# Optimization experiments

Measured on AMD Instinct MI355X. Metric: run time of the kernel, lower is better.

## Reference

```python
import jax, jax.numpy as jnp
import numpy as np

N = 100_000      # nodes in batched candidate graph
P = 150_000      # undirected bonds
E = 2 * P        # directed edges; edge 2i=(u,v), 2i+1=(v,u)
M = 10_000       # tree messages scattered onto edges
DN, DE, DM, DX = 256, 64, 256, 256
ITERS = 3


def setup_inputs() -> dict:
    key = jax.random.key(0)
    ks = jax.random.split(key, 12)
    f_node = jax.random.normal(ks[0], (N, DN), jnp.float32)
    f_edge = jax.random.normal(ks[1], (E, DE), jnp.float32)
    src_p = jax.random.randint(ks[2], (P,), 0, N, dtype=jnp.int32)
    dst_p = jax.random.randint(ks[3], (P,), 0, N, dtype=jnp.int32)
    edge_src = jnp.stack([src_p, dst_p], axis=1).reshape(-1)  # [E]
    edge_dst = jnp.stack([dst_p, src_p], axis=1).reshape(-1)  # [E]
    tree_msg = jax.random.normal(ks[4], (M, DM), jnp.float32)
    tree_tgt = (jnp.arange(M, dtype=jnp.int32) * (E // M))    # unique target edge ids
    s = lambda d: np.float32(1.0 / np.sqrt(d))
    W1 = jax.random.normal(ks[5], (DN, DM), jnp.float32) * s(DN)
    W2 = jax.random.normal(ks[6], (DE, DM), jnp.float32) * s(DE)
    W3 = jax.random.normal(ks[7], (DM, DM), jnp.float32) * s(DM)
    b1 = jnp.zeros((DM,), jnp.float32)
    W4 = jax.random.normal(ks[8], (DN, DX), jnp.float32) * s(DN)
    W5 = jax.random.normal(ks[9], (DM, DX), jnp.float32) * s(DM)
    b2 = jnp.zeros((DX,), jnp.float32)
    return dict(f_node=f_node, f_edge=f_edge, tree_msg=tree_msg,
                W1=W1, W2=W2, W3=W3, b1=b1, W4=W4, W5=W5, b2=b2,
                edge_src=edge_src, edge_dst=edge_dst, tree_tgt=tree_tgt)


def reference(f_node, f_edge, tree_msg, W1, W2, W3, b1, W4, W5, b2,
              edge_src, edge_dst, tree_tgt):
    n_nodes = f_node.shape[0]
    n_edges = f_edge.shape[0]
    d_msg = W3.shape[0]
    # scatter tree messages into per-edge alpha (edata['alpha'])
    alpha = jnp.zeros((n_edges, d_msg), f_node.dtype).at[tree_tgt].set(tree_msg)
    # g1_G static part: W1 f_src + W2 f_edge + b1 (constant across iterations)
    base = f_node[edge_src] @ W1 + f_edge @ W2 + b1  # [E, DM]
    rev = jnp.arange(n_edges) ^ 1  # reverse edge of e (pairs stored consecutively)
    msg = jnp.zeros((n_edges, d_msg), f_node.dtype)
    for _ in range(ITERS):
        # line-graph (backtracking=False) copy_src + sum reduce:
        # sum over incoming edges (w,u) of e=(u,v) excluding w==v
        agg = jax.ops.segment_sum(msg, edge_dst, num_segments=n_nodes)  # [N, DM]
        sum_msg = agg[edge_src] - msg[rev]
        msg = jax.nn.relu(base + (sum_msg + alpha) @ W3)
    # readout: copy_edge + sum per destination node, then g2_G
    node_sum = jax.ops.segment_sum(msg, edge_dst, num_segments=n_nodes)  # [N, DM]
    x = jax.nn.relu(f_node @ W4 + node_sum @ W5 + b2)  # [N, DX]
    return x
```

## Files before the change

### kernel.cpp

```cpp
#include <hip/hip_runtime.h>
#include <hip/hip_bf16.h>

typedef __hip_bfloat16 bf16;
typedef __bf16 bf16x8 __attribute__((ext_vector_type(8)));
typedef __bf16 bf16x4 __attribute__((ext_vector_type(4)));
typedef float f32x4 __attribute__((ext_vector_type(4)));

#define DN_ 256
#define DE_ 64
#define DM_ 256
#define DX_ 256
#define LDA1 264
#define LDA2 72
#define CAP 32


static __device__ __forceinline__ bf16 f2b(float x) { return __float2bfloat16(x); }
static __device__ __forceinline__ float us2f(unsigned short u) {
    return __uint_as_float((unsigned)u << 16);
}

union U16x8 { uint4 u; unsigned short s[8]; };

static __device__ __forceinline__ f32x4 mfma16(bf16x8 a, bf16x8 b, f32x4 c) {
    return __builtin_amdgcn_mfma_f32_16x16x32_bf16(a, b, c, 0, 0, 0);
}

template <int LDA, int KTOT>
static __device__ __forceinline__ void gemm_acc(const bf16* T, const bf16* WT,
                                                f32x4 acc[4][4], int lane, int wave) {
    const int m = lane & 15, quad = lane >> 4;
#pragma unroll
    for (int k0 = 0; k0 < KTOT; k0 += 32) {
        bf16x8 a[4], b[4];
#pragma unroll
        for (int i = 0; i < 4; ++i)
            a[i] = *(const bf16x8*)&T[(i * 16 + m) * LDA + k0 + quad * 8];
#pragma unroll
        for (int j = 0; j < 4; ++j) {
            int n = wave * 64 + j * 16 + m;
            b[j] = *(const bf16x8*)&WT[(size_t)n * KTOT + k0 + quad * 8];
        }
#pragma unroll
        for (int i = 0; i < 4; ++i)
#pragma unroll
            for (int j = 0; j < 4; ++j)
                acc[i][j] = mfma16(b[j], a[i], acc[i][j]);
    }
}

__global__ void __launch_bounds__(256) k_transpose(const float* __restrict__ W,
                                                   bf16* __restrict__ WT, int K, int NC) {
    int i = blockIdx.x * 256 + threadIdx.x;
    if (i < K * NC) {
        int k = i / NC, n = i % NC;
        WT[n * K + k] = f2b(W[i]);
    }
}

__global__ void __launch_bounds__(256) k_cvt(const float* __restrict__ in,
                                             bf16* __restrict__ out, long total) {
    long i = ((long)blockIdx.x * 256 + threadIdx.x) * 8;
    if (i >= total) return;
    float4 v0 = *(const float4*)(in + i);
    float4 v1 = *(const float4*)(in + i + 4);
    bf16x8 b = {(__bf16)v0.x, (__bf16)v0.y, (__bf16)v0.z, (__bf16)v0.w,
                (__bf16)v1.x, (__bf16)v1.y, (__bf16)v1.z, (__bf16)v1.w};
    *(bf16x8*)(out + i) = b;
}

__global__ void __launch_bounds__(256) k_bucket(const int* __restrict__ edst,
                                                int* __restrict__ cnt,
                                                int* __restrict__ slot, int E) {
    int e = blockIdx.x * 256 + threadIdx.x;
    if (e < E) {
        int d = edst[e];
        int pos = atomicAdd(&cnt[d], 1);
        if (pos < CAP) slot[(size_t)d * CAP + pos] = e;
    }
}

__global__ void __launch_bounds__(256) k_invset(const int* __restrict__ tgt,
                                                int* __restrict__ inv, int M) {
    int r = blockIdx.x * 256 + threadIdx.x;
    if (r < M) inv[tgt[r]] = r;
}

__global__ void __launch_bounds__(256) k_aggregate(const bf16* __restrict__ msg,
                                                   const int* __restrict__ cnt,
                                                   const int* __restrict__ slot,
                                                   bf16* __restrict__ agg, int N,
                                                   int relu_in) {
    int wid = (blockIdx.x * 256 + threadIdx.x) >> 6;
    int lane = threadIdx.x & 63;
    if (wid >= N) return;
    int c = cnt[wid];
    if (c > CAP) c = CAP;
    const int* sp = slot + (size_t)wid * CAP;
    float a0 = 0.f, a1 = 0.f, a2 = 0.f, a3 = 0.f;
    if (relu_in) {
        for (int i = 0; i < c; ++i) {
            int e = sp[i];
            ushort4 mv = *(const ushort4*)((const unsigned short*)msg + (size_t)e * DM_ + lane * 4);
            a0 += fmaxf(us2f(mv.x), 0.f); a1 += fmaxf(us2f(mv.y), 0.f);
            a2 += fmaxf(us2f(mv.z), 0.f); a3 += fmaxf(us2f(mv.w), 0.f);
        }
    } else {
        for (int i = 0; i < c; ++i) {
            int e = sp[i];
            ushort4 mv = *(const ushort4*)((const unsigned short*)msg + (size_t)e * DM_ + lane * 4);
            a0 += us2f(mv.x); a1 += us2f(mv.y); a2 += us2f(mv.z); a3 += us2f(mv.w);
        }
    }
    bf16x4 o = {(__bf16)a0, (__bf16)a1, (__bf16)a2, (__bf16)a3};
    *(bf16x4*)(agg + (size_t)wid * DM_ + lane * 4) = o;
}

__global__ void __launch_bounds__(256) k_alpha(const float* __restrict__ tm,
                                               const bf16* __restrict__ W3T,
                                               bf16* __restrict__ alpha3, int M) {
    __shared__ bf16 T[64 * LDA1];
    const int tile0 = blockIdx.x * 64, tid = threadIdx.x;
#pragma unroll
    for (int it = 0; it < 16; ++it) {
        int c = tid + it * 256;
        int r = c >> 6, cc = c & 63;
        int row = tile0 + r;
        if (row >= M) row = 0;
        float4 v = *(const float4*)(tm + (size_t)row * DM_ + cc * 4);
        bf16x4 b = {(__bf16)v.x, (__bf16)v.y, (__bf16)v.z, (__bf16)v.w};
        *(bf16x4*)&T[r * LDA1 + cc * 4] = b;
    }
    __syncthreads();
    const int lane = tid & 63, wave = tid >> 6;
    const int m = lane & 15, quad = lane >> 4;
    f32x4 acc[4][4];
#pragma unroll
    for (int i = 0; i < 4; ++i)
#pragma unroll
        for (int j = 0; j < 4; ++j) acc[i][j] = (f32x4){0.f, 0.f, 0.f, 0.f};
    gemm_acc<LDA1, 256>(T, W3T, acc, lane, wave);
#pragma unroll
    for (int i = 0; i < 4; ++i) {
        int row = tile0 + i * 16 + m;
        if (row < M) {
            size_t rb = (size_t)row * DM_;
#pragma unroll
            for (int j = 0; j < 4; ++j) {
                int c0 = wave * 64 + j * 16 + quad * 4;
                bf16x4 o = {(__bf16)acc[i][j][0], (__bf16)acc[i][j][1],
                            (__bf16)acc[i][j][2], (__bf16)acc[i][j][3]};
                *(bf16x4*)(alpha3 + rb + c0) = o;
            }
        }
    }
}

__global__ void __launch_bounds__(256) k_base(const bf16* __restrict__ fnb,
                                              const float* __restrict__ fedge,
                                              const int* __restrict__ esrc,
                                              const bf16* __restrict__ W1T,
                                              const bf16* __restrict__ W2T,
                                              const float* __restrict__ b1,
                                              const int* __restrict__ inv,
                                              const bf16* __restrict__ alpha3,
                                              bf16* __restrict__ base2, int E) {
    __shared__ bf16 T[64 * LDA1];
    const int tile0 = blockIdx.x * 64, tid = threadIdx.x;
#pragma unroll
    for (int it = 0; it < 8; ++it) {
        int c = tid + it * 256;
        int r = c >> 5, cc = c & 31;
        int e = tile0 + r;
        if (e >= E) e = 0;
        int s = esrc[e];
        *(uint4*)&T[r * LDA1 + cc * 8] =
            *(const uint4*)((const unsigned short*)fnb + (size_t)s * DN_ + cc * 8);
    }
    __syncthreads();
    const int lane = tid & 63, wave = tid >> 6;
    const int m = lane & 15, quad = lane >> 4;
    f32x4 acc[4][4];
#pragma unroll
    for (int i = 0; i < 4; ++i)
#pragma unroll
        for (int j = 0; j < 4; ++j) acc[i][j] = (f32x4){0.f, 0.f, 0.f, 0.f};
    gemm_acc<LDA1, 256>(T, W1T, acc, lane, wave);
    __syncthreads();
#pragma unroll
    for (int it = 0; it < 4; ++it) {
        int c = tid + it * 256;
        int r = c >> 4, cc = c & 15;
        int e = tile0 + r;
        if (e >= E) e = 0;
        float4 v = *(const float4*)(fedge + (size_t)e * DE_ + cc * 4);
        bf16x4 b = {(__bf16)v.x, (__bf16)v.y, (__bf16)v.z, (__bf16)v.w};
        *(bf16x4*)&T[r * LDA2 + cc * 4] = b;
    }
    __syncthreads();
    gemm_acc<LDA2, 64>(T, W2T, acc, lane, wave);
    float4 bj[4];
#pragma unroll
    for (int j = 0; j < 4; ++j)
        bj[j] = *(const float4*)&b1[wave * 64 + j * 16 + quad * 4];
#pragma unroll
    for (int i = 0; i < 4; ++i) {
        int e = tile0 + i * 16 + m;
        if (e < E) {
            int iv = inv[e];
            size_t rb = (size_t)e * DM_;
#pragma unroll
            for (int j = 0; j < 4; ++j) {
                int c0 = wave * 64 + j * 16 + quad * 4;
                float v0 = acc[i][j][0] + bj[j].x;
                float v1 = acc[i][j][1] + bj[j].y;
                float v2 = acc[i][j][2] + bj[j].z;
                float v3 = acc[i][j][3] + bj[j].w;
                if (iv >= 0) {
                    ushort4 al = *(const ushort4*)((const unsigned short*)alpha3 +
                                                   (size_t)iv * DM_ + c0);
                    v0 += us2f(al.x); v1 += us2f(al.y);
                    v2 += us2f(al.z); v3 += us2f(al.w);
                }
                bf16x4 o = {(__bf16)v0, (__bf16)v1, (__bf16)v2, (__bf16)v3};
                *(bf16x4*)(base2 + rb + c0) = o;
            }
        }
    }
}

__global__ void __launch_bounds__(256) k_update(const bf16* __restrict__ agg,
                                                const bf16* __restrict__ base2,
                                                const int* __restrict__ esrc,
                                                const bf16* __restrict__ W3T,
                                                const bf16* __restrict__ msgin,
                                                bf16* __restrict__ msgout, int E,
                                                int relu_in) {
    __shared__ bf16 T[64 * LDA1];
    const int tile0 = blockIdx.x * 64, tid = threadIdx.x;
#pragma unroll
    for (int it = 0; it < 8; ++it) {
        int c = tid + it * 256;
        int r = c >> 5, cc = c & 31;
        int e = tile0 + r;
        int ec = e < E ? e : 0;
        int s = esrc[ec];
        int erev = tile0 + (r ^ 1);
        if (erev >= E) erev = 0;
        U16x8 av, mv;
        av.u = *(const uint4*)((const unsigned short*)agg + (size_t)s * DM_ + cc * 8);
        mv.u = *(const uint4*)((const unsigned short*)msgin + (size_t)erev * DM_ + cc * 8);
        bf16x8 o;
#pragma unroll
        for (int t = 0; t < 8; ++t) {
            float fm = us2f(mv.s[t]);
            if (relu_in) fm = fmaxf(fm, 0.f);
            o[t] = (__bf16)(us2f(av.s[t]) - fm);
        }
        *(bf16x8*)&T[r * LDA1 + cc * 8] = o;
    }
    __syncthreads();
    const int lane = tid & 63, wave = tid >> 6;
    const int m = lane & 15, quad = lane >> 4;
    f32x4 acc[4][4];
#pragma unroll
    for (int i = 0; i < 4; ++i)
#pragma unroll
        for (int j = 0; j < 4; ++j) acc[i][j] = (f32x4){0.f, 0.f, 0.f, 0.f};
    gemm_acc<LDA1, 256>(T, W3T, acc, lane, wave);
#pragma unroll
    for (int i = 0; i < 4; ++i) {
        int e = tile0 + i * 16 + m;
        if (e < E) {
            size_t rb = (size_t)e * DM_;
#pragma unroll
            for (int j = 0; j < 4; ++j) {
                int c0 = wave * 64 + j * 16 + quad * 4;
                ushort4 bv = *(const ushort4*)((const unsigned short*)base2 + rb + c0);
                float v0 = fmaxf(acc[i][j][0] + us2f(bv.x), 0.f);
                float v1 = fmaxf(acc[i][j][1] + us2f(bv.y), 0.f);
                float v2 = fmaxf(acc[i][j][2] + us2f(bv.z), 0.f);
                float v3 = fmaxf(acc[i][j][3] + us2f(bv.w), 0.f);
                bf16x4 o = {(__bf16)v0, (__bf16)v1, (__bf16)v2, (__bf16)v3};
                *(bf16x4*)(msgout + rb + c0) = o;
            }
        }
    }
}

__global__ void __launch_bounds__(256) k_readout(const float* __restrict__ fnode,
                                                 const bf16* __restrict__ agg,
                                                 const bf16* __restrict__ W4T,
                                                 const bf16* __restrict__ W5T,
                                                 const float* __restrict__ b2,
                                                 float* __restrict__ out, int N) {
    __shared__ bf16 T[64 * LDA1];
    const int tile0 = blockIdx.x * 64, tid = threadIdx.x;
#pragma unroll
    for (int it = 0; it < 16; ++it) {
        int c = tid + it * 256;
        int r = c >> 6, cc = c & 63;
        int n = tile0 + r;
        if (n >= N) n = 0;
        float4 v = *(const float4*)(fnode + (size_t)n * DN_ + cc * 4);
        bf16x4 b = {(__bf16)v.x, (__bf16)v.y, (__bf16)v.z, (__bf16)v.w};
        *(bf16x4*)&T[r * LDA1 + cc * 4] = b;
    }
    __syncthreads();
    const int lane = tid & 63, wave = tid >> 6;
    const int m = lane & 15, quad = lane >> 4;
    f32x4 acc[4][4];
#pragma unroll
    for (int i = 0; i < 4; ++i)
#pragma unroll
        for (int j = 0; j < 4; ++j) acc[i][j] = (f32x4){0.f, 0.f, 0.f, 0.f};
    gemm_acc<LDA1, 256>(T, W4T, acc, lane, wave);
    __syncthreads();
#pragma unroll
    for (int it = 0; it < 8; ++it) {
        int c = tid + it * 256;
        int r = c >> 5, cc = c & 31;
        int n = tile0 + r;
        if (n >= N) n = 0;
        *(uint4*)&T[r * LDA1 + cc * 8] =
            *(const uint4*)((const unsigned short*)agg + (size_t)n * DM_ + cc * 8);
    }
    __syncthreads();
    gemm_acc<LDA1, 256>(T, W5T, acc, lane, wave);
    float4 bj[4];
#pragma unroll
    for (int j = 0; j < 4; ++j)
        bj[j] = *(const float4*)&b2[wave * 64 + j * 16 + quad * 4];
#pragma unroll
    for (int i = 0; i < 4; ++i) {
        int n = tile0 + i * 16 + m;
        if (n < N) {
            size_t rb = (size_t)n * DX_;
#pragma unroll
            for (int j = 0; j < 4; ++j) {
                int c0 = wave * 64 + j * 16 + quad * 4;
                float4 o;
                o.x = fmaxf(acc[i][j][0] + bj[j].x, 0.f);
                o.y = fmaxf(acc[i][j][1] + bj[j].y, 0.f);
                o.z = fmaxf(acc[i][j][2] + bj[j].z, 0.f);
                o.w = fmaxf(acc[i][j][3] + bj[j].w, 0.f);
                *(float4*)(out + rb + c0) = o;
            }
        }
    }
}

extern "C" void kernel_launch(void* const* d_in, const int* in_sizes, int n_in,
                              void* d_out, int out_size, void* d_ws, size_t ws_size,
                              hipStream_t stream) {
    const float* f_node   = (const float*)d_in[0];
    const float* f_edge   = (const float*)d_in[1];
    const float* tree_msg = (const float*)d_in[2];
    const float* W1 = (const float*)d_in[3];
    const float* W2 = (const float*)d_in[4];
    const float* W3 = (const float*)d_in[5];
    const float* b1 = (const float*)d_in[6];
    const float* W4 = (const float*)d_in[7];
    const float* W5 = (const float*)d_in[8];
    const float* b2 = (const float*)d_in[9];
    const int* edge_src = (const int*)d_in[10];
    const int* edge_dst = (const int*)d_in[11];
    const int* tree_tgt = (const int*)d_in[12];

    const int N = in_sizes[0] / DN_;
    const int E = in_sizes[1] / DE_;
    const int M = in_sizes[2] / DM_;

    char* ws = (char*)d_ws;
    size_t off = 0;
    bf16* base2 = (bf16*)(ws + off); off += (size_t)E * DM_ * 2;
    bf16* msg   = (bf16*)(ws + off); off += (size_t)E * DM_ * 2;
    bf16* agg   = (bf16*)(ws + off); off += (size_t)N * DM_ * 2;
    int* cnt    = (int*)(ws + off);   off += (size_t)N * 4;
    int* slot   = (int*)(ws + off);   off += (size_t)N * CAP * 4;
    int* inv    = (int*)(ws + off);   off += (size_t)E * 4;
    bf16* alpha3 = (bf16*)(ws + off); off += (size_t)M * DM_ * 2;
    bf16* W1T = (bf16*)(ws + off); off += 256 * 256 * 2;
    bf16* W2T = (bf16*)(ws + off); off += 256 * 64 * 2;
    bf16* W3T = (bf16*)(ws + off); off += 256 * 256 * 2;
    bf16* W4T = (bf16*)(ws + off); off += 256 * 256 * 2;
    bf16* W5T = (bf16*)(ws + off); off += 256 * 256 * 2;
    bf16* fnb = msg;

    k_transpose<<<(256 * 256 + 255) / 256, 256, 0, stream>>>(W1, W1T, 256, 256);
    k_transpose<<<(64 * 256 + 255) / 256, 256, 0, stream>>>(W2, W2T, 64, 256);
    k_transpose<<<(256 * 256 + 255) / 256, 256, 0, stream>>>(W3, W3T, 256, 256);
    k_transpose<<<(256 * 256 + 255) / 256, 256, 0, stream>>>(W4, W4T, 256, 256);
    k_transpose<<<(256 * 256 + 255) / 256, 256, 0, stream>>>(W5, W5T, 256, 256);

    hipMemsetAsync(cnt, 0, (size_t)N * 4, stream);
    hipMemsetAsync(inv, 0xFF, (size_t)E * 4, stream);
    k_bucket<<<(E + 255) / 256, 256, 0, stream>>>(edge_dst, cnt, slot, E);
    k_invset<<<(M + 255) / 256, 256, 0, stream>>>(tree_tgt, inv, M);

    k_cvt<<<(int)(((size_t)N * DN_ / 8 + 255) / 256), 256, 0, stream>>>(
        f_node, fnb, (long)N * DN_);

    k_alpha<<<(M + 63) / 64, 256, 0, stream>>>(tree_msg, W3T, alpha3, M);
    k_base<<<(E + 63) / 64, 256, 0, stream>>>(fnb, f_edge, edge_src, W1T, W2T, b1,
                                              inv, alpha3, base2, E);
    k_aggregate<<<(N + 3) / 4, 256, 0, stream>>>(base2, cnt, slot, agg, N, 1);
    k_update<<<(E + 63) / 64, 256, 0, stream>>>(agg, base2, edge_src, W3T,
                                                base2, msg, E, 1);
    k_aggregate<<<(N + 3) / 4, 256, 0, stream>>>(msg, cnt, slot, agg, N, 0);
    k_update<<<(E + 63) / 64, 256, 0, stream>>>(agg, base2, edge_src, W3T,
                                                msg, msg, E, 0);
    k_aggregate<<<(N + 3) / 4, 256, 0, stream>>>(msg, cnt, slot, agg, N, 0);
    k_readout<<<(N + 63) / 64, 256, 0, stream>>>(f_node, agg, W4T, W5T, b2,
                                                 (float*)d_out, N);
}
```

Baseline: 1.087 ms.

## Apply W3 before aggregation via linearity, fusing gather and update per node

Uses linearity to compute msg@W3 per edge first (k_gemm3). A per-node kernel (k_fuse) then sums the projected incoming messages, subtracts the reverse edge's term, adds base and applies relu, writing each outgoing edge. This removes the separate aggregate buffer pass and the gather of agg by edge source inside the GEMM kernel. It costs an extra E×DM bf16 intermediate buffer and reads each slot list twice. It only runs when the workspace is large enough, otherwise it falls back to the old path.

```diff
diff --git a/kernel.cpp b/kernel.cpp
--- a/kernel.cpp
+++ b/kernel.cpp
@@ -229,6 +229,83 @@
     }
 }
 
+__global__ void __launch_bounds__(256) k_gemm3(const bf16* __restrict__ src,
+                                               const bf16* __restrict__ W3T,
+                                               bf16* __restrict__ m3, int E,
+                                               int relu_in) {
+    __shared__ bf16 T[64 * LDA1];
+    const int tile0 = blockIdx.x * 64, tid = threadIdx.x;
+#pragma unroll
+    for (int it = 0; it < 8; ++it) {
+        int c = tid + it * 256;
+        int r = c >> 5, cc = c & 31;
+        int e = tile0 + r;
+        if (e >= E) e = 0;
+        U16x8 v;
+        v.u = *(const uint4*)((const unsigned short*)src + (size_t)e * DM_ + cc * 8);
+        if (relu_in) {
+#pragma unroll
+            for (int t = 0; t < 8; ++t)
+                if ((short)v.s[t] < 0) v.s[t] = 0;
+        }
+        *(uint4*)&T[r * LDA1 + cc * 8] = v.u;
+    }
+    __syncthreads();
+    const int lane = tid & 63, wave = tid >> 6;
+    const int m = lane & 15, quad = lane >> 4;
+    f32x4 acc[4][4];
+#pragma unroll
+    for (int i = 0; i < 4; ++i)
+#pragma unroll
+        for (int j = 0; j < 4; ++j) acc[i][j] = (f32x4){0.f, 0.f, 0.f, 0.f};
+    gemm_acc<LDA1, 256>(T, W3T, acc, lane, wave);
+#pragma unroll
+    for (int i = 0; i < 4; ++i) {
+        int e = tile0 + i * 16 + m;
+        if (e < E) {
+            size_t rb = (size_t)e * DM_;
+#pragma unroll
+            for (int j = 0; j < 4; ++j) {
+                int c0 = wave * 64 + j * 16 + quad * 4;
+                bf16x4 o = {(__bf16)acc[i][j][0], (__bf16)acc[i][j][1],
+                            (__bf16)acc[i][j][2], (__bf16)acc[i][j][3]};
+                *(bf16x4*)(m3 + rb + c0) = o;
+            }
+        }
+    }
+}
+
+__global__ void __launch_bounds__(256) k_fuse(const bf16* __restrict__ m3,
+                                              const bf16* __restrict__ base2,
+                                              const int* __restrict__ cnt,
+                                              const int* __restrict__ slot,
+                                              bf16* __restrict__ msg, int N) {
+    int wid = (blockIdx.x * 256 + threadIdx.x) >> 6;
+    int lane = threadIdx.x & 63;
+    if (wid >= N) return;
+    int c = cnt[wid];
+    if (c > CAP) c = CAP;
+    const int* sp = slot + (size_t)wid * CAP;
+    float a0 = 0.f, a1 = 0.f, a2 = 0.f, a3 = 0.f;
+    for (int i = 0; i < c; ++i) {
+        int er = sp[i];
+        ushort4 mv = *(const ushort4*)((const unsigned short*)m3 + (size_t)er * DM_ + lane * 4);
+        a0 += us2f(mv.x); a1 += us2f(mv.y); a2 += us2f(mv.z); a3 += us2f(mv.w);
+    }
+    for (int i = 0; i < c; ++i) {
+        int er = sp[i];
+        int e = er ^ 1;
+        ushort4 mv = *(const ushort4*)((const unsigned short*)m3 + (size_t)er * DM_ + lane * 4);
+        ushort4 bv = *(const ushort4*)((const unsigned short*)base2 + (size_t)e * DM_ + lane * 4);
+        float v0 = fmaxf(us2f(bv.x) + a0 - us2f(mv.x), 0.f);
+        float v1 = fmaxf(us2f(bv.y) + a1 - us2f(mv.y), 0.f);
+        float v2 = fmaxf(us2f(bv.z) + a2 - us2f(mv.z), 0.f);
+        float v3 = fmaxf(us2f(bv.w) + a3 - us2f(mv.w), 0.f);
+        bf16x4 o = {(__bf16)v0, (__bf16)v1, (__bf16)v2, (__bf16)v3};
+        *(bf16x4*)(msg + (size_t)e * DM_ + lane * 4) = o;
+    }
+}
+
 __global__ void __launch_bounds__(256) k_update(const bf16* __restrict__ agg,
                                                 const bf16* __restrict__ base2,
                                                 const int* __restrict__ esrc,
@@ -371,11 +448,13 @@
     const int E = in_sizes[1] / DE_;
     const int M = in_sizes[2] / DM_;
 
+    const size_t EB = (size_t)E * DM_ * 2;
+    const size_t NB = (size_t)N * DM_ * 2;
+
     char* ws = (char*)d_ws;
     size_t off = 0;
-    bf16* base2 = (bf16*)(ws + off); off += (size_t)E * DM_ * 2;
-    bf16* msg   = (bf16*)(ws + off); off += (size_t)E * DM_ * 2;
-    bf16* agg   = (bf16*)(ws + off); off += (size_t)N * DM_ * 2;
+    bf16* base2 = (bf16*)(ws + off); off += EB;
+    bf16* msg   = (bf16*)(ws + off); off += EB;
     int* cnt    = (int*)(ws + off);   off += (size_t)N * 4;
     int* slot   = (int*)(ws + off);   off += (size_t)N * CAP * 4;
     int* inv    = (int*)(ws + off);   off += (size_t)E * 4;
@@ -385,6 +464,9 @@
     bf16* W3T = (bf16*)(ws + off); off += 256 * 256 * 2;
     bf16* W4T = (bf16*)(ws + off); off += 256 * 256 * 2;
     bf16* W5T = (bf16*)(ws + off); off += 256 * 256 * 2;
+    const int big = (ws_size - off) >= EB;
+    bf16* m3  = (bf16*)(ws + off);
+    bf16* agg = (bf16*)(ws + off);
     bf16* fnb = msg;
 
     k_transpose<<<(256 * 256 + 255) / 256, 256, 0, stream>>>(W1, W1T, 256, 256);
@@ -404,12 +486,19 @@
     k_alpha<<<(M + 63) / 64, 256, 0, stream>>>(tree_msg, W3T, alpha3, M);
     k_base<<<(E + 63) / 64, 256, 0, stream>>>(fnb, f_edge, edge_src, W1T, W2T, b1,
                                               inv, alpha3, base2, E);
-    k_aggregate<<<(N + 3) / 4, 256, 0, stream>>>(base2, cnt, slot, agg, N, 1);
-    k_update<<<(E + 63) / 64, 256, 0, stream>>>(agg, base2, edge_src, W3T,
-                                                base2, msg, E, 1);
-    k_aggregate<<<(N + 3) / 4, 256, 0, stream>>>(msg, cnt, slot, agg, N, 0);
-    k_update<<<(E + 63) / 64, 256, 0, stream>>>(agg, base2, edge_src, W3T,
-                                                msg, msg, E, 0);
+    if (big) {
+        k_gemm3<<<(E + 63) / 64, 256, 0, stream>>>(base2, W3T, m3, E, 1);
+        k_fuse<<<(N + 3) / 4, 256, 0, stream>>>(m3, base2, cnt, slot, msg, N);
+        k_gemm3<<<(E + 63) / 64, 256, 0, stream>>>(msg, W3T, m3, E, 0);
+        k_fuse<<<(N + 3) / 4, 256, 0, stream>>>(m3, base2, cnt, slot, msg, N);
+    } else {
+        k_aggregate<<<(N + 3) / 4, 256, 0, stream>>>(base2, cnt, slot, agg, N, 1);
+        k_update<<<(E + 63) / 64, 256, 0, stream>>>(agg, base2, edge_src, W3T,
+                                                    base2, msg, E, 1);
+        k_aggregate<<<(N + 3) / 4, 256, 0, stream>>>(msg, cnt, slot, agg, N, 0);
+        k_update<<<(E + 63) / 64, 256, 0, stream>>>(agg, base2, edge_src, W3T,
+                                                    msg, msg, E, 0);
+    }
     k_aggregate<<<(N + 3) / 4, 256, 0, stream>>>(msg, cnt, slot, agg, N, 0);
     k_readout<<<(N + 63) / 64, 256, 0, stream>>>(f_node, agg, W4T, W5T, b2,
                                                  (float*)d_out, N);
```

After: 1.088 ms. Within noise of the previous version (+0.1%).
